# Kernel optimization log

Hardware: AMD Instinct MI355X
Metric: run time of the kernel (lower is better)

Reference implementation:

```python
import jax, jax.numpy as jnp
import numpy as np


def _shift(x, k):
    # roll time axis forward by k, zero-filling the first k steps
    if k == 0:
        return x
    return jnp.pad(x, ((0, 0), (k, 0), (0, 0)))[:, : x.shape[1]]


def _stu_conv(u, v, n):
    # u: (B,L,D), v: (L,K) spectral filters; non-tensordot branch of conv()
    B, L, D = u.shape
    K = v.shape[1]
    sgn = jnp.where(jnp.arange(L) % 2 == 1, -1.0, 1.0).astype(jnp.float32)[None, :, None, None]
    ue = jnp.broadcast_to(u[:, :, None, :], (B, L, K, D)).astype(jnp.float32)
    U = jnp.stack([ue, ue * sgn], axis=-1)                     # (B,L,K,D,2)
    Uf = jnp.fft.rfft(U, n=n, axis=1)
    vf = jnp.fft.rfft(v.astype(jnp.float32)[None, :, :, None, None], n=n, axis=1)
    Uc = jnp.fft.irfft(vf * Uf, n=n, axis=1)[:, :L]            # (B,L,K,D,2)
    U_plus = Uc[..., 0]
    U_minus = Uc[..., 1] * sgn
    return U_plus.astype(u.dtype), U_minus.astype(u.dtype)


def setup_inputs() -> dict:
    key = jax.random.key(0)
    ks = jax.random.split(key, 6)
    B, L, D, K, k_u, k_y = 2, 1024, 512, 16, 3, 2
    u = jax.random.normal(ks[0], (B, L, D), jnp.float32)
    filters = jax.random.normal(ks[1], (L, K), jnp.float32) / np.float32(np.sqrt(L))
    M_u = jax.random.normal(ks[2], (D, k_u, D), jnp.float32) * 0.01
    M_y = jax.random.normal(ks[3], (D, k_y, D), jnp.float32) * 0.01
    M_phi_plus = jax.random.normal(ks[4], (K, D, D), jnp.float32) * 0.01
    M_phi_minus = jax.random.normal(ks[5], (K, D, D), jnp.float32) * 0.01
    return {"u": u, "filters": filters, "M_u": M_u, "M_y": M_y,
            "M_phi_plus": M_phi_plus, "M_phi_minus": M_phi_minus}


def reference(u, filters, M_u, M_y, M_phi_plus, M_phi_minus):
    B, L, D = u.shape
    n = 1 << int(np.ceil(np.log2(2 * L - 1)))  # nearest power of two >= 2L-1
    k_u = M_u.shape[1]
    k_y = M_y.shape[1]

    # FFT-based long convolution with the +/- sign trick
    U_plus, U_minus = _stu_conv(u, filters, n)
    spectral = (jnp.einsum('blkd,kdo->blo', U_plus, M_phi_plus)
                + jnp.einsum('blkd,kdo->blo', U_minus, M_phi_minus))

    # input-AR term of compute_ar_strict: sum_j u[t+1-j] @ M_u[:, j-1].T (shifts 0..k_u-1)
    u_sh = jnp.stack([_shift(u, j - 1) for j in range(1, k_u + 1)], axis=1)  # (B,k_u,L,D)
    y_in = jnp.einsum('bjlf,ijf->bli', u_sh, M_u)

    z = spectral + y_in  # (B,L,D)

    # output-AR recurrence of compute_ar_strict as a scan
    def step(y_buf, z_t):
        y_t = z_t + jnp.einsum('bjf,djf->bd', y_buf, M_y)
        y_buf = jnp.concatenate([y_t[:, None], y_buf[:, :-1]], axis=1)
        return y_buf, y_t

    _, ys = jax.lax.scan(step, jnp.zeros((B, k_y, D), z.dtype), jnp.swapaxes(z, 0, 1))
    return jnp.swapaxes(ys, 0, 1)  # (B,L,D)
```

## Files before the change

### kernel.cpp

```cpp
#include <hip/hip_runtime.h>
#include <hip/hip_bf16.h>


using bf16 = __hip_bfloat16;
typedef __attribute__((ext_vector_type(8))) short bf16x8;
typedef __attribute__((ext_vector_type(4))) float f32x4;

#define B_   2
#define L_   1024
#define D_   512
#define K_   16
#define KT   17920
#define ROWS 2048
#define NTAP 6
#define PBLD 3584
#define SPLITD 16
#define SPLITR 6
#define ZBROWS 1032

#define WAIT_VM6 0x0F76
#define WAIT_VM4 0x0F74
#define WAIT_VM0 0x0F70

__device__ __forceinline__ void gll16(const void* g, void* l) {
    __builtin_amdgcn_global_load_lds(
        (const __attribute__((address_space(1))) unsigned int*)g,
        (__attribute__((address_space(3))) unsigned int*)l, 16, 0, 0);
}

__global__ void prep_all(const float* __restrict__ u, const float* __restrict__ fil,
                         const float* __restrict__ Mu, const float* __restrict__ My,
                         const float* __restrict__ Mp, const float* __restrict__ Mm,
                         bf16* __restrict__ U, bf16* __restrict__ BT,
                         bf16* __restrict__ PB, bf16* __restrict__ W,
                         bf16* __restrict__ Myb, bf16* __restrict__ BTT,
                         bf16* __restrict__ uPT) {
    __shared__ bf16 t[64][72];
    int bid = blockIdx.x, tid = threadIdx.x;
    auto pack4 = [](float4 v) {
        ushort4 o; bf16 h;
        h = __float2bfloat16(v.x); o.x = *(unsigned short*)&h;
        h = __float2bfloat16(v.y); o.y = *(unsigned short*)&h;
        h = __float2bfloat16(v.z); o.z = *(unsigned short*)&h;
        h = __float2bfloat16(v.w); o.w = *(unsigned short*)&h;
        return o;
    };
    if (bid < 3072) {
        int e4 = bid * 256 + tid;
        int r = e4 / 384, rem = e4 % 384;
        int tt = rem >> 7, f = (rem & 127) * 4;
        int b = r >> 10, l = r & 1023;
        float4 v = {0.f, 0.f, 0.f, 0.f};
        if (l >= tt) v = *(const float4*)&u[((size_t)b * L_ + l - tt) * D_ + f];
        *(ushort4*)&U[(size_t)r * KT + 16384 + tt * 512 + f] = pack4(v);
    } else if (bid < 3840) {
        int e4 = (bid - 3072) * 256 + tid;
        int o = e4 / 384, tf4 = (e4 % 384) * 4;
        float4 v = *(const float4*)&Mu[(size_t)o * 1536 + tf4];
        *(ushort4*)&BT[(size_t)o * KT + 16384 + tf4] = pack4(v);
    } else if (bid < 4352) {
        int e4 = (bid - 3840) * 256 + tid;
        int n = e4 >> 8, c4 = (e4 & 255) * 4;
        float4 v;
        if (c4 < 512) {
            v.x = (n == c4) ? 1.f : 0.f;     v.y = (n == c4 + 1) ? 1.f : 0.f;
            v.z = (n == c4 + 2) ? 1.f : 0.f; v.w = (n == c4 + 3) ? 1.f : 0.f;
        } else v = *(const float4*)&My[(size_t)n * 1024 + (c4 - 512)];
        *(ushort4*)&PB[(size_t)n * PBLD + c4] = pack4(v);
    } else if (bid < 5120) {
        int tile = bid - 4352;
        int set = tile >> 8, rem = tile & 255;
        int k = rem >> 4, g = (rem >> 2) & 3, kb = rem & 3;
        for (int idx = tid; idx < 4096; idx += 256) {
            int i = idx >> 5, jp = idx & 31;
            int j = ((jp >> 3) ^ ((i >> 1) & 3)) * 8 + (jp & 7);
            int x = g * 128 + i - kb * 32 - j - (set == 2 ? 1 : 0);
            float v = 0.f;
            if (x >= 0) {
                int row = (set == 0) ? 2 * x : 2 * x + 1;
                v = fil[row * K_ + k];
            }
            W[(size_t)tile * 4096 + idx] = __float2bfloat16(v);
        }
    } else if (bid < 5632) {
        int e4 = (bid - 5120) * 256 + tid;
        float4 v = *(const float4*)&My[(size_t)e4 * 4];
        *(ushort4*)&Myb[(size_t)e4 * 4] = pack4(v);
    } else {
        int tt = bid - 5632;
        int zb = tt >> 6, rem = tt & 63;
        int bx = rem & 7, by = rem >> 3;
        int col = tid & 63, r0 = (tid >> 6) * 16;
        if (zb < 32) {
            int dt = bx * 64, ot = by * 64, c = zb;
            int k = c & 15;
            const float* sp = Mp + (size_t)k * D_ * D_;
            const float* sm = Mm + (size_t)k * D_ * D_;
            float sg = (c < 16) ? 1.f : -1.f;
            for (int i = 0; i < 16; ++i) {
                size_t o_ = (size_t)(dt + r0 + i) * D_ + ot + col;
                t[r0 + i][col] = __float2bfloat16(sp[o_] + sg * sm[o_]);
            }
            __syncthreads();
            for (int i = 0; i < 16; ++i)
                BT[(size_t)(ot + r0 + i) * KT + c * D_ + dt + col] = t[col][r0 + i];
        } else if (zb < 34) {
            int h = zb - 32;
            int dt = bx * 64, ft = by * 64;
            for (int i = 0; i < 16; ++i)
                t[r0 + i][col] = __float2bfloat16(My[(size_t)(dt + r0 + i) * 1024 + (1 - h) * 512 + ft + col]);
            __syncthreads();
            for (int i = 0; i < 16; ++i)
                BTT[(size_t)(ft + r0 + i) * 1024 + h * 512 + dt + col] = t[col][r0 + i];
        } else {
            for (int it = 0; it < 4; ++it) {
                int b = it >> 1, p = it & 1;
                int mt = bx * 64, dt = by * 64;
                __syncthreads();
                for (int i = 0; i < 16; ++i)
                    t[r0 + i][col] = __float2bfloat16(u[((size_t)b * L_ + 2 * (mt + r0 + i) + p) * D_ + dt + col]);
                __syncthreads();
                for (int i = 0; i < 16; ++i)
                    uPT[((size_t)it * 512 + dt + r0 + i) * 512 + mt + col] = t[col][r0 + i];
            }
        }
    }
}

__device__ __forceinline__ void phi_body(
    const bf16* A, int lda, const bf16* BT, int ldb,
    bf16* out, int ldo, int klen, const bf16* add, int lad,
    int row0, int col0, bf16* sA, bf16* sB)
{
    const int tid = threadIdx.x, lane = tid & 63, wave = tid >> 6;
    const int wm = (wave & 1) * 64, wn = (wave >> 1) * 64;
    const int ml = lane & 15, q = lane >> 4;
    const int srow = lane >> 2, scol = (((lane & 3) ^ ((srow >> 1) & 3))) * 8;
    const int swz = ((ml >> 1) & 3);
    f32x4 acc[4][4] = {};

    for (int k = 0; k < klen; k += 32) {
        __syncthreads();
        #pragma unroll
        for (int repi = 0; repi < 2; ++repi) {
            int a = wave + repi * 4;
            gll16(A  + (size_t)(row0 + a * 16 + srow) * lda + k + scol, &sA[a * 512]);
            gll16(BT + (size_t)(col0 + a * 16 + srow) * ldb + k + scol, &sB[a * 512]);
        }
        __syncthreads();
        bf16x8 af[4], bfr[4];
        #pragma unroll
        for (int i = 0; i < 4; ++i)
            af[i] = *(const bf16x8*)&sA[(wm + i * 16 + ml) * 32 + (q ^ swz) * 8];
        #pragma unroll
        for (int j = 0; j < 4; ++j)
            bfr[j] = *(const bf16x8*)&sB[(wn + j * 16 + ml) * 32 + (q ^ swz) * 8];
        #pragma unroll
        for (int i = 0; i < 4; ++i)
            #pragma unroll
            for (int j = 0; j < 4; ++j)
                acc[i][j] = __builtin_amdgcn_mfma_f32_16x16x32_bf16(af[i], bfr[j], acc[i][j], 0, 0, 0);
    }
    #pragma unroll
    for (int i = 0; i < 4; ++i)
        #pragma unroll
        for (int j = 0; j < 4; ++j)
            #pragma unroll
            for (int reg = 0; reg < 4; ++reg) {
                int r = row0 + wm + i * 16 + q * 4 + reg;
                int cc = col0 + wn + j * 16 + ml;
                float v = acc[i][j][reg];
                if (add) v += __bfloat162float(add[(size_t)r * lad + cc]);
                out[(size_t)r * ldo + cc] = __float2bfloat16(v);
            }
}

__global__ void k_ztaps(const bf16* __restrict__ partD, float* __restrict__ z,
                        bf16* __restrict__ zbuf, bf16* PB, const bf16* BTT) {
    __shared__ bf16 sA[4096];
    __shared__ bf16 sB[4096];
    int bid = blockIdx.x;
    if (bid < 32) {
        int row0 = (bid & 3) * 128, col0 = (bid >> 2) * 128;
        phi_body(PB + 3 * 512, PBLD, BTT, 1024, PB + 5 * 512, PBLD, 1024,
                 nullptr, 0, row0, col0, sA, sB);
        return;
    }
    if (bid == 32) {
        ushort4 z4 = {0, 0, 0, 0};
        for (int i = 0; i < 8; ++i) {
            int e4 = i * 256 + threadIdx.x;
            int b = e4 >> 10, rem = e4 & 1023;
            int g = rem >> 7, c4 = (rem & 127) * 4;
            *(ushort4*)&zbuf[(size_t)(b * ZBROWS + g) * 512 + c4] = z4;
        }
        return;
    }
    int t = (bid - 33) * 256 + threadIdx.x;
    int r = t >> 7, f4 = (t & 127) * 4;
    const ushort4* p = (const ushort4*)partD;
    float4 s = {0.f, 0.f, 0.f, 0.f};
    #pragma unroll
    for (int c = 0; c < SPLITD; ++c) {
        ushort4 v = p[(size_t)c * (ROWS * D_ / 4) + t];
        s.x += __uint_as_float((unsigned)v.x << 16);
        s.y += __uint_as_float((unsigned)v.y << 16);
        s.z += __uint_as_float((unsigned)v.z << 16);
        s.w += __uint_as_float((unsigned)v.w << 16);
    }
    ((float4*)z)[t] = s;
    ushort4 zb4;
    { bf16 h;
      h = __float2bfloat16(s.x); zb4.x = *(unsigned short*)&h;
      h = __float2bfloat16(s.y); zb4.y = *(unsigned short*)&h;
      h = __float2bfloat16(s.z); zb4.z = *(unsigned short*)&h;
      h = __float2bfloat16(s.w); zb4.w = *(unsigned short*)&h; }
    int b = r >> 10, li = r & 1023;
    *(ushort4*)&zbuf[(size_t)(b * ZBROWS + 8 + li) * 512 + f4] = zb4;
}

__global__ void reduce_out(const float* __restrict__ z, const bf16* __restrict__ partR,
                           float* __restrict__ out) {
    int t = blockIdx.x * 256 + threadIdx.x;
    if (t >= ROWS * D_ / 4) return;
    float4 s = ((const float4*)z)[t];
    const ushort4* p = (const ushort4*)partR;
    #pragma unroll
    for (int c = 0; c < SPLITR; ++c) {
        ushort4 v = p[(size_t)c * (ROWS * D_ / 4) + t];
        s.x += __uint_as_float((unsigned)v.x << 16);
        s.y += __uint_as_float((unsigned)v.y << 16);
        s.z += __uint_as_float((unsigned)v.z << 16);
        s.w += __uint_as_float((unsigned)v.w << 16);
    }
    ((float4*)out)[t] = s;
}

__global__ __launch_bounds__(256, 3) void conv_misc(
    const bf16* __restrict__ W, const bf16* __restrict__ uPT,
    bf16* __restrict__ U,
    const bf16* PB, const bf16* BTT, const bf16* Myb)
{
    __shared__ bf16 sA[3][4096];
    __shared__ bf16 sB[3][4096];
    const int z = blockIdx.z;
    if (z < 3) {
        int row0 = blockIdx.x * 128, col0 = blockIdx.y * 128;
        bf16* BTTw = (bf16*)BTT; bf16* PBw = (bf16*)PB;
        if (z == 0)
            phi_body(PB, PBLD, BTT, 1024, PBw + 2 * 512, PBLD, 1024,
                     nullptr, 0, row0, col0, &sA[0][0], &sB[0][0]);
        else if (z == 1)
            phi_body(BTT + 512, 1024, Myb + 512, 1024,
                     BTTw + (size_t)512 * 1024, 1024, 512,
                     nullptr, 0, row0, col0, &sA[0][0], &sB[0][0]);
        else
            phi_body(BTT + 512, 1024, Myb, 1024,
                     BTTw + (size_t)512 * 1024 + 512, 1024, 512,
                     BTT, 1024, row0, col0, &sA[0][0], &sB[0][0]);
        return;
    }
    const int zc = z - 3;
    const int mt = 3 - blockIdx.x, dt = blockIdx.y * 128;
    const int t = zc & 3, b = (zc >> 2) & 1, k = zc >> 3;
    const int pb_ = t & 1;
    const int p = (t & 1) ^ (t >> 1);
    const int set = (t < 2) ? 0 : (t == 2 ? 1 : 2);
    const int ch = (t < 2) ? k : 16 + k;
    const int plane = b * 2 + pb_;
    const int tid = threadIdx.x, lane = tid & 63, wave = tid >> 6;
    const int wm = (wave & 1) * 64, wn = (wave >> 1) * 64;
    const int ml = lane & 15, q = lane >> 4;
    const int srow = lane >> 2, scol = (((lane & 3) ^ ((srow >> 1) & 3))) * 8;
    const int swz = ((ml >> 1) & 3);
    f32x4 acc[4][4] = {};
    const int n = (mt + 1) * 4;

    const bf16* bB0 = uPT + ((size_t)plane * 512 + dt + wave * 16       + srow) * 512 + scol;
    const bf16* bB1 = uPT + ((size_t)plane * 512 + dt + (wave + 4) * 16 + srow) * 512 + scol;
    const bf16* wbase = W + ((size_t)(set * 16 + k) * 16) * 4096;
    auto stage = [&](int s, int buf) {
        const bf16* wt = wbase + ((size_t)((mt - (s >> 2)) * 4 + (s & 3))) * 4096;
        gll16(wt + wave * 512 + lane * 8, &sA[buf][wave * 512]);
        gll16(wt + (wave + 4) * 512 + lane * 8, &sA[buf][(wave + 4) * 512]);
        gll16(bB0 + s * 32, &sB[buf][wave * 512]);
        gll16(bB1 + s * 32, &sB[buf][(wave + 4) * 512]);
    };
    auto compute = [&](int c) {
        bf16x8 af[4], bfr[4];
        #pragma unroll
        for (int i = 0; i < 4; ++i)
            af[i] = *(const bf16x8*)&sA[c][(wm + i * 16 + ml) * 32 + (q ^ swz) * 8];
        #pragma unroll
        for (int j = 0; j < 4; ++j)
            bfr[j] = *(const bf16x8*)&sB[c][(wn + j * 16 + ml) * 32 + (q ^ swz) * 8];
        #pragma unroll
        for (int i = 0; i < 4; ++i)
            #pragma unroll
            for (int j = 0; j < 4; ++j)
                acc[i][j] = __builtin_amdgcn_mfma_f32_16x16x32_bf16(af[i], bfr[j], acc[i][j], 0, 0, 0);
    };
    stage(0, 0); stage(1, 1);
    int c = 0, nb = 2;
    for (int i = 0; i < n - 1; ++i) {
        __builtin_amdgcn_s_waitcnt(WAIT_VM4);
        __builtin_amdgcn_s_barrier();
        if (i + 2 < n) stage(i + 2, nb);
        compute(c);
        c = (c == 2) ? 0 : c + 1; nb = (nb == 2) ? 0 : nb + 1;
    }
    __builtin_amdgcn_s_waitcnt(WAIT_VM0);
    __builtin_amdgcn_s_barrier();
    compute(c);

    #pragma unroll
    for (int i = 0; i < 4; ++i)
        #pragma unroll
        for (int j = 0; j < 4; ++j)
            #pragma unroll
            for (int reg = 0; reg < 4; ++reg) {
                int m = mt * 128 + wm + i * 16 + q * 4 + reg;
                int l = 2 * m + p;
                int d = dt + wn + j * 16 + ml;
                U[(size_t)(b * L_ + l) * KT + ch * 512 + d] = __float2bfloat16(acc[i][j][reg]);
            }
}

__global__ __launch_bounds__(256, 2) void gemm_k(
    const bf16* __restrict__ A, int lda, int k_chunk,
    const bf16* __restrict__ BT, int ldb,
    bf16* __restrict__ part,
    const bf16* __restrict__ zbuf,
    int swzgrid, const bf16* PB, const bf16* BTT)
{
    __shared__ bf16 sA[3][4096];
    __shared__ bf16 sB[3][8192];
    int row0, col0, zz;
    if (swzgrid) {
        int id = blockIdx.x;
        if (id < 32) {
            int r0_ = (id & 3) * 128, c0_ = (id >> 2) * 128;
            phi_body(PB + 512, PBLD, BTT, 1024, (bf16*)PB + 3 * 512, PBLD, 1024,
                     nullptr, 0, r0_, c0_, &sA[0][0], &sB[0][0]);
            return;
        }
        id -= 32;
        int xcd = id & 7, n_ = id >> 3;
        zz = xcd + 8 * (n_ >> 5);
        int rem = n_ & 31;
        row0 = (rem >> 1) * 128;
        col0 = (rem & 1) * 256;
    } else {
        row0 = blockIdx.x * 128; col0 = blockIdx.y * 256; zz = blockIdx.z;
    }
    const int tid = threadIdx.x, lane = tid & 63, wave = tid >> 6;
    const int wm = (wave & 1) * 64, wn = (wave >> 1) * 128;
    const int ml = lane & 15, q = lane >> 4;
    const int srow = lane >> 2, scol = (((lane & 3) ^ ((srow >> 1) & 3))) * 8;
    const int swz = ((ml >> 1) & 3);
    f32x4 acc[4][8] = {};

    const bf16* Abase; int alda, n, k0;
    if (zbuf) {
        int s = 1 + zz;
        int b = row0 >> 10, li0 = row0 & 1023;
        Abase = zbuf + ((size_t)(b * ZBROWS + 8 + li0 - s)) * 512;
        alda = 512; n = 16; k0 = zz * 512;
    } else {
        Abase = A + (size_t)row0 * lda + (size_t)zz * k_chunk;
        alda = lda; n = k_chunk >> 5; k0 = zz * k_chunk;
    }
    const bf16* bA0 = Abase + (size_t)(wave * 16 + srow) * alda + scol;
    const bf16* bA1 = Abase + (size_t)((wave + 4) * 16 + srow) * alda + scol;
    const bf16* bB[4];
    #pragma unroll
    for (int r = 0; r < 4; ++r)
        bB[r] = BT + (size_t)(col0 + (wave + r * 4) * 16 + srow) * ldb + k0 + scol;

    auto stage = [&](int s, int buf) {
        gll16(bA0 + s * 32, &sA[buf][wave * 512]);
        gll16(bA1 + s * 32, &sA[buf][(wave + 4) * 512]);
        #pragma unroll
        for (int r = 0; r < 4; ++r)
            gll16(bB[r] + s * 32, &sB[buf][(wave + r * 4) * 512]);
    };
    auto compute = [&](int c) {
        bf16x8 af[4], bfr[8];
        #pragma unroll
        for (int i = 0; i < 4; ++i)
            af[i] = *(const bf16x8*)&sA[c][(wm + i * 16 + ml) * 32 + (q ^ swz) * 8];
        #pragma unroll
        for (int j = 0; j < 8; ++j)
            bfr[j] = *(const bf16x8*)&sB[c][(wn + j * 16 + ml) * 32 + (q ^ swz) * 8];
        #pragma unroll
        for (int i = 0; i < 4; ++i)
            #pragma unroll
            for (int j = 0; j < 8; ++j)
                acc[i][j] = __builtin_amdgcn_mfma_f32_16x16x32_bf16(af[i], bfr[j], acc[i][j], 0, 0, 0);
    };
    stage(0, 0); stage(1, 1);
    int c = 0, nb = 2;
    for (int i = 0; i < n - 1; ++i) {
        __builtin_amdgcn_s_waitcnt(WAIT_VM6);
        __builtin_amdgcn_s_barrier();
        if (i + 2 < n) stage(i + 2, nb);
        compute(c);
        c = (c == 2) ? 0 : c + 1; nb = (nb == 2) ? 0 : nb + 1;
    }
    __builtin_amdgcn_s_waitcnt(WAIT_VM0);
    __builtin_amdgcn_s_barrier();
    compute(c);

    bf16* o = part + (size_t)zz * ROWS * D_;
    #pragma unroll
    for (int i = 0; i < 4; ++i)
        #pragma unroll
        for (int j = 0; j < 8; ++j)
            #pragma unroll
            for (int reg = 0; reg < 4; ++reg) {
                int r = row0 + wm + i * 16 + q * 4 + reg;
                int cc = col0 + wn + j * 16 + ml;
                o[(size_t)r * D_ + cc] = __float2bfloat16(acc[i][j][reg]);
            }
}

extern "C" void kernel_launch(void* const* d_in, const int* in_sizes, int n_in,
                              void* d_out, int out_size, void* d_ws, size_t ws_size,
                              hipStream_t stream) {
    const float* u   = (const float*)d_in[0];
    const float* fil = (const float*)d_in[1];
    const float* Mu  = (const float*)d_in[2];
    const float* My  = (const float*)d_in[3];
    const float* Mp  = (const float*)d_in[4];
    const float* Mm  = (const float*)d_in[5];
    float* out = (float*)d_out;

    char* ws = (char*)d_ws;
    size_t off = 0;
    auto alloc = [&](size_t bytes) { void* p = ws + off; off = (off + bytes + 255) & ~(size_t)255; return p; };
    bf16*  U    = (bf16*) alloc((size_t)ROWS * KT * 2);
    bf16*  BT   = (bf16*) alloc((size_t)512 * KT * 2);
    bf16*  PB   = (bf16*) alloc((size_t)512 * PBLD * 2);
    bf16*  BTT  = (bf16*) alloc((size_t)1024 * 1024 * 2);
    bf16*  Myb  = (bf16*) alloc((size_t)512 * 1024 * 2);
    float* z    = (float*)alloc((size_t)ROWS * D_ * 4);
    bf16*  zb   = (bf16*) alloc((size_t)B_ * ZBROWS * 512 * 2);
    char*  region = (char*)alloc((size_t)SPLITD * ROWS * D_ * 2);
    bf16*  W    = (bf16*)region;
    bf16*  uPT  = (bf16*)(region + (size_t)768 * 4096 * 2);
    bf16*  partD = (bf16*)region;
    bf16*  partR = (bf16*)region;

    prep_all<<<7872, 256, 0, stream>>>(u, fil, Mu, My, Mp, Mm,
                                       U, BT, PB, W, Myb, BTT, uPT);

    conv_misc<<<dim3(4, 4, 131), 256, 0, stream>>>(W, uPT, U, PB, BTT, Myb);

    gemm_k<<<544, 256, 0, stream>>>(U, KT, KT / SPLITD, BT, KT, partD,
                                    nullptr, 1, PB, BTT);

    k_ztaps<<<1057, 256, 0, stream>>>(partD, z, zb, PB, BTT);

    gemm_k<<<dim3(16, 2, SPLITR), 256, 0, stream>>>(nullptr, 0, 512,
                                                    PB + 512, PBLD, partR,
                                                    zb, 0, nullptr, nullptr);

    reduce_out<<<(ROWS * D_ / 4 + 255) / 256, 256, 0, stream>>>(z, partR, out);
}
```

Baseline: 253.4 us.

## Split GEMM into 128x128 tiles with paired-stage pipeline and halve split-K

The generic gemm_k is split into dedicated gemm_d and gemm_r kernels built on a shared 128x128 tile routine. The old 3-buffer, one-step-ahead pipeline becomes a 4-buffer scheme that stages two K-steps at a time and waits for all loads before each pair. The main GEMM's split-K factor drops from 16 to 8, which halves the partial buffers that k_ztaps must reduce. The smaller tile lowers data reuse per block and raises per-block operand traffic, and the full wait weakens load/compute overlap.

```diff
diff --git a/kernel.cpp b/kernel.cpp
--- a/kernel.cpp
+++ b/kernel.cpp
@@ -14,11 +14,10 @@
 #define ROWS 2048
 #define NTAP 6
 #define PBLD 3584
-#define SPLITD 16
+#define SPLITD 8
 #define SPLITR 6
 #define ZBROWS 1032
 
-#define WAIT_VM6 0x0F76
 #define WAIT_VM4 0x0F74
 #define WAIT_VM0 0x0F70
 
@@ -326,102 +325,99 @@
             }
 }
 
-__global__ __launch_bounds__(256, 2) void gemm_k(
-    const bf16* __restrict__ A, int lda, int k_chunk,
-    const bf16* __restrict__ BT, int ldb,
-    bf16* __restrict__ part,
-    const bf16* __restrict__ zbuf,
-    int swzgrid, const bf16* PB, const bf16* BTT)
+__device__ __forceinline__ void mm128_pair(
+    const bf16* Abase, int alda, const bf16* Bbase, int ldb, int n,
+    bf16* o, int row0, int col0, bf16 (*sA)[4096], bf16 (*sB)[4096])
 {
-    __shared__ bf16 sA[3][4096];
-    __shared__ bf16 sB[3][8192];
-    int row0, col0, zz;
-    if (swzgrid) {
-        int id = blockIdx.x;
-        if (id < 32) {
-            int r0_ = (id & 3) * 128, c0_ = (id >> 2) * 128;
-            phi_body(PB + 512, PBLD, BTT, 1024, (bf16*)PB + 3 * 512, PBLD, 1024,
-                     nullptr, 0, r0_, c0_, &sA[0][0], &sB[0][0]);
-            return;
-        }
-        id -= 32;
-        int xcd = id & 7, n_ = id >> 3;
-        zz = xcd + 8 * (n_ >> 5);
-        int rem = n_ & 31;
-        row0 = (rem >> 1) * 128;
-        col0 = (rem & 1) * 256;
-    } else {
-        row0 = blockIdx.x * 128; col0 = blockIdx.y * 256; zz = blockIdx.z;
-    }
     const int tid = threadIdx.x, lane = tid & 63, wave = tid >> 6;
-    const int wm = (wave & 1) * 64, wn = (wave >> 1) * 128;
+    const int wm = (wave & 1) * 64, wn = (wave >> 1) * 64;
     const int ml = lane & 15, q = lane >> 4;
     const int srow = lane >> 2, scol = (((lane & 3) ^ ((srow >> 1) & 3))) * 8;
     const int swz = ((ml >> 1) & 3);
-    f32x4 acc[4][8] = {};
-
-    const bf16* Abase; int alda, n, k0;
-    if (zbuf) {
-        int s = 1 + zz;
-        int b = row0 >> 10, li0 = row0 & 1023;
-        Abase = zbuf + ((size_t)(b * ZBROWS + 8 + li0 - s)) * 512;
-        alda = 512; n = 16; k0 = zz * 512;
-    } else {
-        Abase = A + (size_t)row0 * lda + (size_t)zz * k_chunk;
-        alda = lda; n = k_chunk >> 5; k0 = zz * k_chunk;
-    }
+    f32x4 acc[4][4] = {};
+
     const bf16* bA0 = Abase + (size_t)(wave * 16 + srow) * alda + scol;
     const bf16* bA1 = Abase + (size_t)((wave + 4) * 16 + srow) * alda + scol;
-    const bf16* bB[4];
-    #pragma unroll
-    for (int r = 0; r < 4; ++r)
-        bB[r] = BT + (size_t)(col0 + (wave + r * 4) * 16 + srow) * ldb + k0 + scol;
-
-    auto stage = [&](int s, int buf) {
+    const bf16* bB0 = Bbase + (size_t)(wave * 16 + srow) * ldb + scol;
+    const bf16* bB1 = Bbase + (size_t)((wave + 4) * 16 + srow) * ldb + scol;
+    auto stage = [&](int s) {
+        int buf = s & 3;
         gll16(bA0 + s * 32, &sA[buf][wave * 512]);
         gll16(bA1 + s * 32, &sA[buf][(wave + 4) * 512]);
-        #pragma unroll
-        for (int r = 0; r < 4; ++r)
-            gll16(bB[r] + s * 32, &sB[buf][(wave + r * 4) * 512]);
+        gll16(bB0 + s * 32, &sB[buf][wave * 512]);
+        gll16(bB1 + s * 32, &sB[buf][(wave + 4) * 512]);
     };
     auto compute = [&](int c) {
-        bf16x8 af[4], bfr[8];
+        bf16x8 af[4], bfr[4];
         #pragma unroll
         for (int i = 0; i < 4; ++i)
             af[i] = *(const bf16x8*)&sA[c][(wm + i * 16 + ml) * 32 + (q ^ swz) * 8];
         #pragma unroll
-        for (int j = 0; j < 8; ++j)
+        for (int j = 0; j < 4; ++j)
             bfr[j] = *(const bf16x8*)&sB[c][(wn + j * 16 + ml) * 32 + (q ^ swz) * 8];
         #pragma unroll
         for (int i = 0; i < 4; ++i)
             #pragma unroll
-            for (int j = 0; j < 8; ++j)
+            for (int j = 0; j < 4; ++j)
                 acc[i][j] = __builtin_amdgcn_mfma_f32_16x16x32_bf16(af[i], bfr[j], acc[i][j], 0, 0, 0);
     };
-    stage(0, 0); stage(1, 1);
-    int c = 0, nb = 2;
-    for (int i = 0; i < n - 1; ++i) {
-        __builtin_amdgcn_s_waitcnt(WAIT_VM6);
+    stage(0); stage(1);
+    const int npair = n >> 1;
+    for (int p = 0; p < npair; ++p) {
+        __builtin_amdgcn_s_waitcnt(WAIT_VM0);
         __builtin_amdgcn_s_barrier();
-        if (i + 2 < n) stage(i + 2, nb);
-        compute(c);
-        c = (c == 2) ? 0 : c + 1; nb = (nb == 2) ? 0 : nb + 1;
-    }
-    __builtin_amdgcn_s_waitcnt(WAIT_VM0);
-    __builtin_amdgcn_s_barrier();
-    compute(c);
-
-    bf16* o = part + (size_t)zz * ROWS * D_;
+        if (2 * p + 2 < n) { stage(2 * p + 2); stage(2 * p + 3); }
+        compute((2 * p) & 3);
+        compute((2 * p + 1) & 3);
+    }
     #pragma unroll
     for (int i = 0; i < 4; ++i)
         #pragma unroll
-        for (int j = 0; j < 8; ++j)
+        for (int j = 0; j < 4; ++j)
             #pragma unroll
             for (int reg = 0; reg < 4; ++reg) {
                 int r = row0 + wm + i * 16 + q * 4 + reg;
                 int cc = col0 + wn + j * 16 + ml;
                 o[(size_t)r * D_ + cc] = __float2bfloat16(acc[i][j][reg]);
             }
+}
+
+__global__ __launch_bounds__(256, 2) void gemm_d(
+    const bf16* __restrict__ U, const bf16* __restrict__ BT,
+    bf16* __restrict__ part, const bf16* PB, const bf16* BTT)
+{
+    __shared__ bf16 sA[4][4096];
+    __shared__ bf16 sB[4][4096];
+    int id = blockIdx.x;
+    if (id < 32) {
+        int r0_ = (id & 3) * 128, c0_ = (id >> 2) * 128;
+        phi_body(PB + 512, PBLD, BTT, 1024, (bf16*)PB + 3 * 512, PBLD, 1024,
+                 nullptr, 0, r0_, c0_, &sA[0][0], &sB[0][0]);
+        return;
+    }
+    id -= 32;
+    const int xcd = id & 7, n_ = id >> 3;
+    const int zz = xcd;
+    const int row0 = (n_ >> 2) * 128, col0 = (n_ & 3) * 128;
+    const int kc = KT / SPLITD;
+    mm128_pair(U + (size_t)row0 * KT + (size_t)zz * kc, KT,
+               BT + (size_t)col0 * KT + (size_t)zz * kc, KT,
+               kc >> 5, part + (size_t)zz * ROWS * D_, row0, col0, sA, sB);
+}
+
+__global__ __launch_bounds__(256, 2) void gemm_r(
+    const bf16* __restrict__ zbuf, const bf16* __restrict__ BT,
+    bf16* __restrict__ part)
+{
+    __shared__ bf16 sA[4][4096];
+    __shared__ bf16 sB[4][4096];
+    const int row0 = blockIdx.x * 128, col0 = blockIdx.y * 128;
+    const int zz = blockIdx.z;
+    const int s = 1 + zz;
+    const int b = row0 >> 10, li0 = row0 & 1023;
+    mm128_pair(zbuf + ((size_t)(b * ZBROWS + 8 + li0 - s)) * 512, 512,
+               BT + (size_t)col0 * PBLD + (size_t)zz * 512, PBLD,
+               16, part + (size_t)zz * ROWS * D_, row0, col0, sA, sB);
 }
 
 extern "C" void kernel_launch(void* const* d_in, const int* in_sizes, int n_in,
@@ -445,7 +441,7 @@
     bf16*  Myb  = (bf16*) alloc((size_t)512 * 1024 * 2);
     float* z    = (float*)alloc((size_t)ROWS * D_ * 4);
     bf16*  zb   = (bf16*) alloc((size_t)B_ * ZBROWS * 512 * 2);
-    char*  region = (char*)alloc((size_t)SPLITD * ROWS * D_ * 2);
+    char*  region = (char*)alloc((size_t)16 * ROWS * D_ * 2);
     bf16*  W    = (bf16*)region;
     bf16*  uPT  = (bf16*)(region + (size_t)768 * 4096 * 2);
     bf16*  partD = (bf16*)region;
@@ -456,14 +452,11 @@
 
     conv_misc<<<dim3(4, 4, 131), 256, 0, stream>>>(W, uPT, U, PB, BTT, Myb);
 
-    gemm_k<<<544, 256, 0, stream>>>(U, KT, KT / SPLITD, BT, KT, partD,
-                                    nullptr, 1, PB, BTT);
+    gemm_d<<<544, 256, 0, stream>>>(U, BT, partD, PB, BTT);
 
     k_ztaps<<<1057, 256, 0, stream>>>(partD, z, zb, PB, BTT);
 
-    gemm_k<<<dim3(16, 2, SPLITR), 256, 0, stream>>>(nullptr, 0, 512,
-                                                    PB + 512, PBLD, partR,
-                                                    zb, 0, nullptr, nullptr);
+    gemm_r<<<dim3(16, 4, SPLITR), 256, 0, stream>>>(zb, PB + 512, partR);
 
     reduce_out<<<(ROWS * D_ / 4 + 255) / 256, 256, 0, stream>>>(z, partR, out);
 }
```

Result: slower. 258.6 us (+2.1%).
